# Kernel optimization log

Measured on AMD Instinct MI355X. Metric: run time of the kernel, lower is better.

## Reference

```python
import jax, jax.numpy as jnp
import numpy as np

IN_FEATURES = 1024
OUT_FEATURES = 1024
NUM_TOKENS = 1024
RANK = 32


def setup_inputs() -> dict:
    key = jax.random.key(0)
    ks = jax.random.split(key, 7)
    std = 1.0 / np.sqrt(IN_FEATURES)
    x = jax.random.normal(ks[0], (4, 2048, IN_FEATURES), dtype=jnp.float32)
    key_tokens = std * jax.random.normal(ks[1], (NUM_TOKENS, IN_FEATURES), dtype=jnp.float32)
    value_tokens = std * jax.random.normal(ks[2], (NUM_TOKENS, OUT_FEATURES), dtype=jnp.float32)
    key_down = std * jax.random.normal(ks[3], (IN_FEATURES, RANK), dtype=jnp.float32)
    key_up = std * jax.random.normal(ks[4], (RANK, IN_FEATURES), dtype=jnp.float32)
    value_down = std * jax.random.normal(ks[5], (OUT_FEATURES, RANK), dtype=jnp.float32)
    value_up = std * jax.random.normal(ks[6], (RANK, OUT_FEATURES), dtype=jnp.float32)
    return {"x": x, "key_tokens": key_tokens, "value_tokens": value_tokens,
            "key_down": key_down, "key_up": key_up,
            "value_down": value_down, "value_up": value_up}


def _mod_softmax(attn):
    # scale each row by sqrt(last_dim) / ||row||_2, then GELU
    n = attn.shape[-1]
    norm = jnp.sqrt(jnp.sum(attn * attn, axis=-1, keepdims=True))
    return jax.nn.gelu(attn * (jnp.asarray(n, attn.dtype) ** 0.5) / norm, approximate=False)


def reference(x, key_tokens, value_tokens, key_down, key_up, value_down, value_up):
    key_transformed = jax.nn.gelu((key_tokens @ key_down) @ key_up, approximate=False)
    value_transformed = jax.nn.gelu((value_tokens @ value_down) @ value_up, approximate=False)
    combined_keys = jnp.concatenate([key_tokens, key_transformed], axis=0)      # [2T, in]
    combined_values = jnp.concatenate([value_tokens, value_transformed], axis=0)  # [2T, out]
    similarity = jnp.einsum('bsd,td->bst', x, combined_keys)  # [B, S, 2T]
    weights = _mod_softmax(similarity)
    return jnp.einsum('bst,te->bse', weights, combined_values)  # [B, S, out]
```

## Files before the change

kernel.cpp:

```cpp
#include <hip/hip_runtime.h>

#define IN_F 1024
#define OUT_F 1024
#define NT 1024
#define RANK 32
#define M_TOT 8192
#define N2T 2048

typedef __attribute__((ext_vector_type(8))) short short8;
typedef __attribute__((ext_vector_type(4))) float f32x4;
typedef __attribute__((ext_vector_type(8))) unsigned short ushort8;

__device__ __forceinline__ float geluf(float x) {
  return 0.5f * x * (1.0f + erff(x * 0.7071067811865476f));
}
__device__ __forceinline__ unsigned short f2bf(float f) {
  unsigned x = __float_as_uint(f);
  return (unsigned short)((x + 0x7fffu + ((x >> 16) & 1u)) >> 16);
}
__device__ __forceinline__ float bf2f(unsigned short u) {
  return __uint_as_float(((unsigned)u) << 16);
}


__global__ void down_proj_kernel(const float* __restrict__ kt, const float* __restrict__ kd,
                                 const float* __restrict__ vt, const float* __restrict__ vd,
                                 float* __restrict__ tmpK, float* __restrict__ tmpV) {
  __shared__ float rowbuf[IN_F];
  __shared__ float part[8][32];
  const int row = blockIdx.x & (NT - 1);
  const int mat = blockIdx.x >> 10;
  const float* T = mat ? vt : kt;
  const float* D = mat ? vd : kd;
  const int tid = threadIdx.x;
  *(f32x4*)(rowbuf + tid * 4) = *(const f32x4*)(T + (size_t)row * IN_F + tid * 4);
  __syncthreads();
  const int c = tid & 31;
  const int kc = tid >> 5;
  float s = 0.f;
#pragma unroll 4
  for (int k = kc * 128; k < kc * 128 + 128; ++k) s += rowbuf[k] * D[k * RANK + c];
  part[kc][c] = s;
  __syncthreads();
  if (tid < 32) {
    float acc = 0.f;
#pragma unroll
    for (int i = 0; i < 8; ++i) acc += part[i][tid];
    (mat ? tmpV : tmpK)[row * RANK + tid] = acc;
  }
}

__global__ __launch_bounds__(256) void upK_kernel(
    const float* __restrict__ tmpK, const float* __restrict__ key_up,
    unsigned short* __restrict__ Kb) {
  __shared__ float ldsT[32 * 33];
  __shared__ float ldsU[32 * 64];
  const int tid = threadIdx.x;
  const int t0 = (blockIdx.x >> 4) * 32;
  const int d0 = (blockIdx.x & 15) * 64;
  {
    int row = tid >> 3, col = (tid & 7) * 4;
    f32x4 v = *(const f32x4*)(tmpK + (size_t)(t0 + row) * RANK + col);
#pragma unroll
    for (int j = 0; j < 4; ++j) ldsT[row * 33 + col + j] = v[j];
  }
#pragma unroll
  for (int s = 0; s < 2; ++s) {
    int idx = s * 1024 + tid * 4;
    int r = idx >> 6, cc = idx & 63;
    *(f32x4*)(ldsU + idx) = *(const f32x4*)(key_up + (size_t)r * IN_F + d0 + cc);
  }
  __syncthreads();
  const int lane = tid & 63;
  const int w = tid >> 6;
  float acc[8];
#pragma unroll
  for (int i = 0; i < 8; ++i) acc[i] = 0.f;
#pragma unroll
  for (int r = 0; r < RANK; ++r) {
    float wv = ldsU[r * 64 + lane];
#pragma unroll
    for (int i = 0; i < 8; ++i) acc[i] += ldsT[(w * 8 + i) * 33 + r] * wv;
  }
#pragma unroll
  for (int i = 0; i < 8; ++i) {
    int t = t0 + w * 8 + i;
    Kb[(size_t)(NT + t) * IN_F + d0 + lane] = f2bf(geluf(acc[i]));
  }
}

__global__ __launch_bounds__(256) void upV_kernel(
    const float* __restrict__ tmpV, const float* __restrict__ value_up,
    unsigned short* __restrict__ VbT) {
  __shared__ float ldsT[64 * 33];
  __shared__ float ldsU[32 * 32];
  const int tid = threadIdx.x;
  const int t0 = (blockIdx.x >> 5) * 64;
  const int e0 = (blockIdx.x & 31) * 32;
#pragma unroll
  for (int s = 0; s < 2; ++s) {
    int idx = s * 1024 + tid * 4;
    int row = idx >> 5, col = idx & 31;
    f32x4 v = *(const f32x4*)(tmpV + (size_t)(t0 + row) * RANK + col);
#pragma unroll
    for (int j = 0; j < 4; ++j) ldsT[row * 33 + col + j] = v[j];
  }
  {
    int r = tid >> 3, col = (tid & 7) * 4;
    *(f32x4*)(ldsU + r * 32 + col) = *(const f32x4*)(value_up + (size_t)r * OUT_F + e0 + col);
  }
  __syncthreads();
  const int lane = tid & 63;
  const int w = tid >> 6;
  float acc[8];
#pragma unroll
  for (int i = 0; i < 8; ++i) acc[i] = 0.f;
#pragma unroll
  for (int r = 0; r < RANK; ++r) {
    float uv = ldsT[lane * 33 + r];
#pragma unroll
    for (int i = 0; i < 8; ++i) acc[i] += uv * ldsU[r * 32 + w * 8 + i];
  }
#pragma unroll
  for (int i = 0; i < 8; ++i) {
    int e = e0 + w * 8 + i;
    VbT[(size_t)e * N2T + NT + t0 + lane] = f2bf(geluf(acc[i]));
  }
}

__global__ void vcopy_kernel(const float* __restrict__ vt, unsigned short* __restrict__ VbT) {
  __shared__ float tile[64][65];
  int tid = threadIdx.x;
  int bt = blockIdx.x & 15;
  int be = blockIdx.x >> 4;
  int t0 = bt * 64, e0 = be * 64;
#pragma unroll 1
  for (int it = 0; it < 16; ++it) {
    int tt = it * 4 + (tid >> 6);
    int ee = tid & 63;
    tile[tt][ee] = vt[(size_t)(t0 + tt) * OUT_F + e0 + ee];
  }
  __syncthreads();
#pragma unroll 1
  for (int it = 0; it < 16; ++it) {
    int ee = it * 4 + (tid >> 6);
    int tt = tid & 63;
    VbT[(size_t)(e0 + ee) * N2T + t0 + tt] = f2bf(tile[tt][ee]);
  }
}

__global__ void xcast_kernel(const float* __restrict__ x, unsigned short* __restrict__ xb) {
  int base = (blockIdx.x * blockDim.x + threadIdx.x) * 8;
  f32x4 a = *(const f32x4*)(x + base);
  f32x4 b = *(const f32x4*)(x + base + 4);
  ushort8 o;
  o[0] = f2bf(a[0]); o[1] = f2bf(a[1]); o[2] = f2bf(a[2]); o[3] = f2bf(a[3]);
  o[4] = f2bf(b[0]); o[5] = f2bf(b[1]); o[6] = f2bf(b[2]); o[7] = f2bf(b[3]);
  *(ushort8*)(xb + base) = o;
}

__global__ void gelu_kernel(unsigned short* __restrict__ S, const float* __restrict__ rowsq) {
  int base = (blockIdx.x * blockDim.x + threadIdx.x) * 8;
  int row = base >> 11;
  float scale = sqrtf(2048.0f / rowsq[row]);
  ushort8 v = *(const ushort8*)(S + base);
  ushort8 o;
#pragma unroll
  for (int i = 0; i < 8; ++i) o[i] = f2bf(geluf(bf2f(v[i]) * scale));
  *(ushort8*)(S + base) = o;
}

#define BARRB __builtin_amdgcn_s_barrier()

template <int BN, int KDIM, int NDIM, int DO_SIM>
__global__ __launch_bounds__(512, 2) void gemm2p_kernel(
    const unsigned short* __restrict__ A, const unsigned short* __restrict__ Bm,
    void* __restrict__ Cout, float* __restrict__ rowsq) {
  constexpr int NFRAG = BN / 64;
  constexpr int NH = NFRAG / 2;
  constexpr int LB = BN / 128;
  constexpr int ABUFE = 16384;
  constexpr int BBUFE = BN * 64;
  constexpr int nTN = NDIM / BN;
  constexpr int nkt = KDIM / 64;
  __shared__ unsigned short lds[2 * ABUFE + 2 * BBUFE];

  const int tid = threadIdx.x;
  const int l = tid & 63;
  const int wid = tid >> 6;
  const int wr = wid >> 2;
  const int wc = wid & 3;

  const int nwg = gridDim.x;
  const int cpx = nwg >> 3;
  const int wg = (blockIdx.x & 7) * cpx + (blockIdx.x >> 3);
  const int bx = wg % nTN;
  const int by = wg / nTN;
  const int rowBase = by * 256;
  const int colBase = bx * BN;

  const unsigned short* aSrc[2]; int aLds[2];
#pragma unroll
  for (int j = 0; j < 2; ++j) {
    int slot = j * 512 + tid;
    int rin = slot >> 3;
    int cs = (slot & 7) ^ (rin & 7);
    aSrc[j] = A + (size_t)(rowBase + rin) * KDIM + cs * 8;
    aLds[j] = slot * 8;
  }
  const unsigned short* bSrc[LB]; int bLds[LB];
#pragma unroll
  for (int j = 0; j < LB; ++j) {
    int slot = j * 512 + tid;
    int rin = slot >> 3;
    int cs = (slot & 7) ^ (rin & 7);
    bSrc[j] = Bm + (size_t)(colBase + rin) * KDIM + cs * 8;
    bLds[j] = slot * 8;
  }

#define STAGE_A(u, b, kt) { _Pragma("unroll") for (int j = 0; j < 2; ++j) \
    __builtin_amdgcn_global_load_lds( \
      (const __attribute__((address_space(1))) void*)(aSrc[j] + (size_t)(u) * 128 * KDIM + (kt) * 64), \
      (__attribute__((address_space(3))) void*)(lds + (b) * ABUFE + (u) * 8192 + aLds[j]), 16, 0, 0); }
#define STAGE_B(u, b, kt) { _Pragma("unroll") for (int j = 0; j < LB; ++j) \
    __builtin_amdgcn_global_load_lds( \
      (const __attribute__((address_space(1))) void*)(bSrc[j] + (size_t)(u) * (BN / 2) * KDIM + (kt) * 64), \
      (__attribute__((address_space(3))) void*)(lds + 2 * ABUFE + (b) * BBUFE + (u) * (BBUFE / 2) + bLds[j]), 16, 0, 0); }

  const int kb0 = (l >> 4) * 16;
  const int sw = (l & 7) << 4;
  const int lr = l & 15;

  f32x4 acc[8][NFRAG];
#pragma unroll
  for (int m = 0; m < 8; ++m)
#pragma unroll
    for (int n = 0; n < NFRAG; ++n) acc[m][n] = (f32x4){0.f, 0.f, 0.f, 0.f};

  short8 a[4][2], b0[NH][2], b1[NH][2];

#define LDA(mh, bb_) { _Pragma("unroll") for (int i = 0; i < 4; ++i) { \
    int row = ((mh) * 4 + i) * 32 + wr * 16 + lr; \
    const char* pp = (const char*)lds + (bb_) * 32768 + row * 128; \
    a[i][0] = *(const short8*)(pp + ((0 + kb0) ^ sw)); \
    a[i][1] = *(const short8*)(pp + ((64 + kb0) ^ sw)); } }
#define LDB(dst, nh, bb_) { _Pragma("unroll") for (int i = 0; i < NH; ++i) { \
    int row = ((nh) * NH + i) * 64 + wc * 16 + lr; \
    const char* pp = (const char*)lds + 2 * ABUFE * 2 + (bb_) * BBUFE * 2 + row * 128; \
    dst[i][0] = *(const short8*)(pp + ((0 + kb0) ^ sw)); \
    dst[i][1] = *(const short8*)(pp + ((64 + kb0) ^ sw)); } }
#define DO_MFMA(mh, nh, bb) { _Pragma("unroll") for (int kk = 0; kk < 2; ++kk) \
    _Pragma("unroll") for (int i = 0; i < 4; ++i) \
    _Pragma("unroll") for (int nn = 0; nn < NH; ++nn) \
      acc[(mh) * 4 + i][(nh) * NH + nn] = __builtin_amdgcn_mfma_f32_16x16x32_bf16( \
          a[i][kk], bb[nn][kk], acc[(mh) * 4 + i][(nh) * NH + nn], 0, 0, 0); }

  STAGE_A(0, 0, 0); STAGE_A(1, 0, 0); STAGE_B(0, 0, 0); STAGE_B(1, 0, 0);
  STAGE_A(0, 1, 1); STAGE_B(0, 1, 1); STAGE_B(1, 1, 1);
  if constexpr (LB == 2) { asm volatile("s_waitcnt vmcnt(6)" ::: "memory"); }
  else                   { asm volatile("s_waitcnt vmcnt(4)" ::: "memory"); }
  BARRB;

  for (int t = 0; t < nkt; ++t) {
    const int buf = t & 1;
    LDA(0, buf); LDB(b0, 0, buf); LDB(b1, 1, buf);
    if (t + 1 < nkt) STAGE_A(1, buf ^ 1, t + 1);
    BARRB;
    __builtin_amdgcn_s_setprio(1);
    DO_MFMA(0, 0, b0); DO_MFMA(0, 1, b1);
    __builtin_amdgcn_s_setprio(0);
    BARRB;
    LDA(1, buf);
    if (t + 2 < nkt) { STAGE_A(0, buf, t + 2); STAGE_B(0, buf, t + 2); STAGE_B(1, buf, t + 2); }
    BARRB;
    __builtin_amdgcn_s_setprio(1);
    DO_MFMA(1, 1, b1); DO_MFMA(1, 0, b0);
    __builtin_amdgcn_s_setprio(0);
    if constexpr (LB == 2) { asm volatile("s_waitcnt vmcnt(6)" ::: "memory"); }
    else                   { asm volatile("s_waitcnt vmcnt(4)" ::: "memory"); }
    BARRB;
  }

  const int cq = l >> 4;
  const int cc = l & 15;
  if constexpr (DO_SIM) {
    unsigned short* Sb = (unsigned short*)Cout;
#pragma unroll
    for (int m = 0; m < 8; ++m) {
#pragma unroll
      for (int j = 0; j < 4; ++j) {
        int gr = rowBase + m * 32 + wr * 16 + cq * 4 + j;
        float ss = 0.f;
#pragma unroll
        for (int n = 0; n < NFRAG; ++n) {
          float v = acc[m][n][j];
          ss += v * v;
          Sb[(size_t)gr * NDIM + colBase + n * 64 + wc * 16 + cc] = f2bf(v);
        }
        ss += __shfl_xor(ss, 1, 64);
        ss += __shfl_xor(ss, 2, 64);
        ss += __shfl_xor(ss, 4, 64);
        ss += __shfl_xor(ss, 8, 64);
        if (cc == 0) atomicAdd(&rowsq[gr], ss);
      }
    }
  } else {
    float* Co = (float*)Cout;
#pragma unroll
    for (int m = 0; m < 8; ++m) {
#pragma unroll
      for (int j = 0; j < 4; ++j) {
        int gr = rowBase + m * 32 + wr * 16 + cq * 4 + j;
#pragma unroll
        for (int n = 0; n < NFRAG; ++n)
          Co[(size_t)gr * NDIM + colBase + n * 64 + wc * 16 + cc] = acc[m][n][j];
      }
    }
  }
#undef STAGE_A
#undef STAGE_B
#undef LDA
#undef LDB
#undef DO_MFMA
}


extern "C" void kernel_launch(void* const* d_in, const int* in_sizes, int n_in,
                              void* d_out, int out_size, void* d_ws, size_t ws_size,
                              hipStream_t stream) {
  (void)in_sizes; (void)n_in; (void)out_size; (void)ws_size;
  const float* x            = (const float*)d_in[0];
  const float* key_tokens   = (const float*)d_in[1];
  const float* value_tokens = (const float*)d_in[2];
  const float* key_down     = (const float*)d_in[3];
  const float* key_up       = (const float*)d_in[4];
  const float* value_down   = (const float*)d_in[5];
  const float* value_up     = (const float*)d_in[6];

  char* ws = (char*)d_ws;
  unsigned short* xb  = (unsigned short*)(ws);
  unsigned short* Kb  = (unsigned short*)(ws + 16777216);
  unsigned short* VbT = (unsigned short*)(ws + 20971520);
  unsigned short* S   = (unsigned short*)(ws + 25165824);
  float* tmpK  = (float*)(ws + 58720256);
  float* tmpV  = (float*)(ws + 58851328);
  float* rowsq = (float*)(ws + 58982400);

  hipMemsetAsync(rowsq, 0, M_TOT * sizeof(float), stream);
  down_proj_kernel<<<2 * NT, 256, 0, stream>>>(key_tokens, key_down, value_tokens, value_down, tmpK, tmpV);
  xcast_kernel<<<(NT * IN_F) / (256 * 8), 256, 0, stream>>>(key_tokens, Kb);
  upK_kernel<<<512, 256, 0, stream>>>(tmpK, key_up, Kb);
  vcopy_kernel<<<256, 256, 0, stream>>>(value_tokens, VbT);
  upV_kernel<<<512, 256, 0, stream>>>(tmpV, value_up, VbT);
  xcast_kernel<<<(M_TOT * IN_F) / (256 * 8), 256, 0, stream>>>(x, xb);
  gemm2p_kernel<256, IN_F, N2T, 1><<<256, 512, 0, stream>>>(xb, Kb, (void*)S, rowsq);
  gelu_kernel<<<(M_TOT * N2T) / (256 * 8), 256, 0, stream>>>(S, rowsq);
  gemm2p_kernel<128, N2T, OUT_F, 0><<<256, 512, 0, stream>>>(S, VbT, d_out, nullptr);
}
```

Baseline: 147.3 us.

## Fuse norm-scale GELU into second GEMM A-load and merge prep kernels

```diff
diff --git a/kernel.cpp b/kernel.cpp
--- a/kernel.cpp
+++ b/kernel.cpp
@@ -50,14 +50,25 @@
   }
 }
 
-__global__ __launch_bounds__(256) void upK_kernel(
-    const float* __restrict__ tmpK, const float* __restrict__ key_up,
-    unsigned short* __restrict__ Kb) {
+__global__ __launch_bounds__(256) void kprep_kernel(
+    const float* __restrict__ key_tokens, const float* __restrict__ key_up,
+    const float* __restrict__ tmpK, unsigned short* __restrict__ Kb) {
   __shared__ float ldsT[32 * 33];
   __shared__ float ldsU[32 * 64];
   const int tid = threadIdx.x;
-  const int t0 = (blockIdx.x >> 4) * 32;
-  const int d0 = (blockIdx.x & 15) * 64;
+  if (blockIdx.x < 512) {
+    int base = (blockIdx.x * 256 + tid) * 8;
+    f32x4 a = *(const f32x4*)(key_tokens + base);
+    f32x4 b = *(const f32x4*)(key_tokens + base + 4);
+    ushort8 o;
+    o[0] = f2bf(a[0]); o[1] = f2bf(a[1]); o[2] = f2bf(a[2]); o[3] = f2bf(a[3]);
+    o[4] = f2bf(b[0]); o[5] = f2bf(b[1]); o[6] = f2bf(b[2]); o[7] = f2bf(b[3]);
+    *(ushort8*)(Kb + base) = o;
+    return;
+  }
+  const int bid = blockIdx.x - 512;
+  const int t0 = (bid >> 4) * 32;
+  const int d0 = (bid & 15) * 64;
   {
     int row = tid >> 3, col = (tid & 7) * 4;
     f32x4 v = *(const f32x4*)(tmpK + (size_t)(t0 + row) * RANK + col);
@@ -89,14 +100,35 @@
   }
 }
 
-__global__ __launch_bounds__(256) void upV_kernel(
-    const float* __restrict__ tmpV, const float* __restrict__ value_up,
-    unsigned short* __restrict__ VbT) {
-  __shared__ float ldsT[64 * 33];
+__global__ __launch_bounds__(256) void vprep_kernel(
+    const float* __restrict__ vt, const float* __restrict__ value_up,
+    const float* __restrict__ tmpV, unsigned short* __restrict__ VbT) {
+  __shared__ float tile[64][65];
+  const int tid = threadIdx.x;
+  if (blockIdx.x < 256) {
+    int bt = blockIdx.x & 15;
+    int be = blockIdx.x >> 4;
+    int t0 = bt * 64, e0 = be * 64;
+#pragma unroll 1
+    for (int it = 0; it < 16; ++it) {
+      int tt = it * 4 + (tid >> 6);
+      int ee = tid & 63;
+      tile[tt][ee] = vt[(size_t)(t0 + tt) * OUT_F + e0 + ee];
+    }
+    __syncthreads();
+#pragma unroll 1
+    for (int it = 0; it < 16; ++it) {
+      int ee = it * 4 + (tid >> 6);
+      int tt = tid & 63;
+      VbT[(size_t)(e0 + ee) * N2T + t0 + tt] = f2bf(tile[tt][ee]);
+    }
+    return;
+  }
+  const int bid = blockIdx.x - 256;
+  float* ldsT = &tile[0][0];
   __shared__ float ldsU[32 * 32];
-  const int tid = threadIdx.x;
-  const int t0 = (blockIdx.x >> 5) * 64;
-  const int e0 = (blockIdx.x & 31) * 32;
+  const int t0 = (bid >> 5) * 64;
+  const int e0 = (bid & 31) * 32;
 #pragma unroll
   for (int s = 0; s < 2; ++s) {
     int idx = s * 1024 + tid * 4;
@@ -125,27 +157,6 @@
   for (int i = 0; i < 8; ++i) {
     int e = e0 + w * 8 + i;
     VbT[(size_t)e * N2T + NT + t0 + lane] = f2bf(geluf(acc[i]));
-  }
-}
-
-__global__ void vcopy_kernel(const float* __restrict__ vt, unsigned short* __restrict__ VbT) {
-  __shared__ float tile[64][65];
-  int tid = threadIdx.x;
-  int bt = blockIdx.x & 15;
-  int be = blockIdx.x >> 4;
-  int t0 = bt * 64, e0 = be * 64;
-#pragma unroll 1
-  for (int it = 0; it < 16; ++it) {
-    int tt = it * 4 + (tid >> 6);
-    int ee = tid & 63;
-    tile[tt][ee] = vt[(size_t)(t0 + tt) * OUT_F + e0 + ee];
-  }
-  __syncthreads();
-#pragma unroll 1
-  for (int it = 0; it < 16; ++it) {
-    int ee = it * 4 + (tid >> 6);
-    int tt = tid & 63;
-    VbT[(size_t)(e0 + ee) * N2T + t0 + tt] = f2bf(tile[tt][ee]);
   }
 }
 
@@ -157,17 +168,6 @@
   o[0] = f2bf(a[0]); o[1] = f2bf(a[1]); o[2] = f2bf(a[2]); o[3] = f2bf(a[3]);
   o[4] = f2bf(b[0]); o[5] = f2bf(b[1]); o[6] = f2bf(b[2]); o[7] = f2bf(b[3]);
   *(ushort8*)(xb + base) = o;
-}
-
-__global__ void gelu_kernel(unsigned short* __restrict__ S, const float* __restrict__ rowsq) {
-  int base = (blockIdx.x * blockDim.x + threadIdx.x) * 8;
-  int row = base >> 11;
-  float scale = sqrtf(2048.0f / rowsq[row]);
-  ushort8 v = *(const ushort8*)(S + base);
-  ushort8 o;
-#pragma unroll
-  for (int i = 0; i < 8; ++i) o[i] = f2bf(geluf(bf2f(v[i]) * scale));
-  *(ushort8*)(S + base) = o;
 }
 
 #define BARRB __builtin_amdgcn_s_barrier()
@@ -324,6 +324,148 @@
 #undef DO_MFMA
 }
 
+#define FBARR asm volatile("s_barrier" ::: "memory")
+#define FLGKM0 asm volatile("s_waitcnt lgkmcnt(0)" ::: "memory")
+
+__global__ __launch_bounds__(512, 2) void gemm2f_kernel(
+    const unsigned short* __restrict__ S, const float* __restrict__ rowsq,
+    const unsigned short* __restrict__ Bm, float* __restrict__ Co) {
+  constexpr int KDIM = N2T;
+  constexpr int NDIM = OUT_F;
+  constexpr int BN = 128;
+  constexpr int ABUFE = 16384;
+  constexpr int BBUFE = BN * 64;
+  constexpr int nTN = NDIM / BN;
+  constexpr int nkt = KDIM / 64;
+  __shared__ unsigned short lds[2 * ABUFE + 2 * BBUFE];
+
+  const int tid = threadIdx.x;
+  const int l = tid & 63;
+  const int wid = tid >> 6;
+  const int wr = wid >> 2;
+  const int wc = wid & 3;
+
+  const int nwg = gridDim.x;
+  const int cpx = nwg >> 3;
+  const int wg = (blockIdx.x & 7) * cpx + (blockIdx.x >> 3);
+  const int bx = wg % nTN;
+  const int by = wg / nTN;
+  const int rowBase = by * 256;
+  const int colBase = bx * BN;
+
+  const unsigned short* agp[4]; int albyte[4]; float ascale[4];
+#pragma unroll
+  for (int c = 0; c < 4; ++c) {
+    int slot = c * 512 + tid;
+    int rin = slot >> 3;
+    int cch = slot & 7;
+    agp[c] = S + (size_t)(rowBase + rin) * KDIM + cch * 8;
+    albyte[c] = rin * 128 + ((cch * 16) ^ ((rin & 7) << 4));
+    ascale[c] = sqrtf(2048.0f / rowsq[rowBase + rin]);
+  }
+  const unsigned short* bSrc0; int bLds0;
+  {
+    int slot = tid;
+    int rin = slot >> 3;
+    int cs = (slot & 7) ^ (rin & 7);
+    bSrc0 = Bm + (size_t)(colBase + rin) * KDIM + cs * 8;
+    bLds0 = slot * 8;
+  }
+
+#define F_STAGE_B(u, b, kt) \
+    __builtin_amdgcn_global_load_lds( \
+      (const __attribute__((address_space(1))) void*)(bSrc0 + (size_t)(u) * 64 * KDIM + (kt) * 64), \
+      (__attribute__((address_space(3))) void*)(lds + 2 * ABUFE + (b) * BBUFE + (u) * (BBUFE / 2) + bLds0), 16, 0, 0);
+#define F_ALOAD(c, tk) areg##c = *(const ushort8*)(agp[c] + (size_t)(tk) * 64);
+#define F_XFORM(c, tk) { \
+    ushort8 v_ = areg##c; \
+    ushort8 o_; \
+    _Pragma("unroll") for (int i_ = 0; i_ < 8; ++i_) \
+      o_[i_] = f2bf(geluf(bf2f(v_[i_]) * ascale[c])); \
+    *(ushort8*)((char*)lds + (((tk) & 1) * (ABUFE * 2)) + albyte[c]) = o_; }
+
+  const int kb0 = (l >> 4) * 16;
+  const int sw = (l & 7) << 4;
+  const int lr = l & 15;
+
+  f32x4 acc[8][2];
+#pragma unroll
+  for (int m = 0; m < 8; ++m)
+#pragma unroll
+    for (int n = 0; n < 2; ++n) acc[m][n] = (f32x4){0.f, 0.f, 0.f, 0.f};
+
+  short8 a[4][2], b0[2], b1[2];
+  ushort8 areg0, areg1, areg2, areg3;
+
+#define F_LDA(mh, bb_) { _Pragma("unroll") for (int i = 0; i < 4; ++i) { \
+    int row = ((mh) * 4 + i) * 32 + wr * 16 + lr; \
+    const char* pp = (const char*)lds + (bb_) * 32768 + row * 128; \
+    a[i][0] = *(const short8*)(pp + ((0 + kb0) ^ sw)); \
+    a[i][1] = *(const short8*)(pp + ((64 + kb0) ^ sw)); } }
+#define F_LDB(dst, nh, bb_) { \
+    int row = (nh) * 64 + wc * 16 + lr; \
+    const char* pp = (const char*)lds + 2 * ABUFE * 2 + (bb_) * BBUFE * 2 + row * 128; \
+    dst[0] = *(const short8*)(pp + ((0 + kb0) ^ sw)); \
+    dst[1] = *(const short8*)(pp + ((64 + kb0) ^ sw)); }
+#define F_MFMA(mh, nh, bb) { _Pragma("unroll") for (int kk = 0; kk < 2; ++kk) \
+    _Pragma("unroll") for (int i = 0; i < 4; ++i) \
+      acc[(mh) * 4 + i][(nh)] = __builtin_amdgcn_mfma_f32_16x16x32_bf16( \
+          a[i][kk], bb[kk], acc[(mh) * 4 + i][(nh)], 0, 0, 0); }
+
+  F_STAGE_B(0, 0, 0); F_STAGE_B(1, 0, 0);
+  F_ALOAD(0, 0); F_ALOAD(1, 0); F_ALOAD(2, 0); F_ALOAD(3, 0);
+  F_STAGE_B(0, 1, 1); F_STAGE_B(1, 1, 1);
+  asm volatile("s_waitcnt vmcnt(2)" ::: "memory");
+  F_XFORM(0, 0); F_XFORM(1, 0); F_XFORM(2, 0); F_XFORM(3, 0);
+  F_ALOAD(0, 1); F_ALOAD(1, 1);
+  FLGKM0;
+  FBARR;
+
+  for (int t = 0; t < nkt; ++t) {
+    const int buf = t & 1;
+    F_LDA(0, buf); F_LDB(b0, 0, buf); F_LDB(b1, 1, buf);
+    if (t + 1 < nkt) { F_ALOAD(2, t + 1); F_ALOAD(3, t + 1); }
+    FBARR;
+    __builtin_amdgcn_s_setprio(1);
+    F_MFMA(0, 0, b0); F_MFMA(0, 1, b1);
+    __builtin_amdgcn_s_setprio(0);
+    if (t + 1 < nkt) { F_XFORM(0, t + 1); F_XFORM(1, t + 1); }
+    FLGKM0;
+    FBARR;
+    F_LDA(1, buf);
+    if (t + 2 < nkt) {
+      F_STAGE_B(0, buf, t + 2); F_STAGE_B(1, buf, t + 2);
+      F_ALOAD(0, t + 2); F_ALOAD(1, t + 2);
+    }
+    FBARR;
+    __builtin_amdgcn_s_setprio(1);
+    F_MFMA(1, 1, b1); F_MFMA(1, 0, b0);
+    __builtin_amdgcn_s_setprio(0);
+    if (t + 1 < nkt) { F_XFORM(2, t + 1); F_XFORM(3, t + 1); }
+    FLGKM0;
+    FBARR;
+  }
+
+  const int cq = l >> 4;
+  const int cc = l & 15;
+#pragma unroll
+  for (int m = 0; m < 8; ++m) {
+#pragma unroll
+    for (int j = 0; j < 4; ++j) {
+      int gr = rowBase + m * 32 + wr * 16 + cq * 4 + j;
+#pragma unroll
+      for (int n = 0; n < 2; ++n)
+        Co[(size_t)gr * NDIM + colBase + n * 64 + wc * 16 + cc] = acc[m][n][j];
+    }
+  }
+#undef F_STAGE_B
+#undef F_ALOAD
+#undef F_XFORM
+#undef F_LDA
+#undef F_LDB
+#undef F_MFMA
+}
+
 
 extern "C" void kernel_launch(void* const* d_in, const int* in_sizes, int n_in,
                               void* d_out, int out_size, void* d_ws, size_t ws_size,
@@ -348,12 +490,9 @@
 
   hipMemsetAsync(rowsq, 0, M_TOT * sizeof(float), stream);
   down_proj_kernel<<<2 * NT, 256, 0, stream>>>(key_tokens, key_down, value_tokens, value_down, tmpK, tmpV);
-  xcast_kernel<<<(NT * IN_F) / (256 * 8), 256, 0, stream>>>(key_tokens, Kb);
-  upK_kernel<<<512, 256, 0, stream>>>(tmpK, key_up, Kb);
-  vcopy_kernel<<<256, 256, 0, stream>>>(value_tokens, VbT);
-  upV_kernel<<<512, 256, 0, stream>>>(tmpV, value_up, VbT);
+  kprep_kernel<<<1024, 256, 0, stream>>>(key_tokens, key_up, tmpK, Kb);
+  vprep_kernel<<<768, 256, 0, stream>>>(value_tokens, value_up, tmpV, VbT);
   xcast_kernel<<<(M_TOT * IN_F) / (256 * 8), 256, 0, stream>>>(x, xb);
   gemm2p_kernel<256, IN_F, N2T, 1><<<256, 512, 0, stream>>>(xb, Kb, (void*)S, rowsq);
-  gelu_kernel<<<(M_TOT * N2T) / (256 * 8), 256, 0, stream>>>(S, rowsq);
-  gemm2p_kernel<128, N2T, OUT_F, 0><<<256, 512, 0, stream>>>(S, VbT, d_out, nullptr);
-}
+  gemm2f_kernel<<<256, 512, 0, stream>>>(S, rowsq, VbT, (float*)d_out);
+}
```

New measurement: 224.2 us. +52.2%, slower.

## Fuse prep kernels and fold row-norm GELU into similarity GEMM via grid sync

Applied to the files above, without the earlier changes.

```diff
diff --git a/kernel.cpp b/kernel.cpp
--- a/kernel.cpp
+++ b/kernel.cpp
@@ -1,4 +1,5 @@
 #include <hip/hip_runtime.h>
+#include <hip/hip_cooperative_groups.h>
 
 #define IN_F 1024
 #define OUT_F 1024
@@ -25,14 +26,16 @@
 
 __global__ void down_proj_kernel(const float* __restrict__ kt, const float* __restrict__ kd,
                                  const float* __restrict__ vt, const float* __restrict__ vd,
-                                 float* __restrict__ tmpK, float* __restrict__ tmpV) {
+                                 float* __restrict__ tmpK, float* __restrict__ tmpV,
+                                 float* __restrict__ rowsq) {
   __shared__ float rowbuf[IN_F];
   __shared__ float part[8][32];
+  const int tid = threadIdx.x;
+  if (blockIdx.x < 32) rowsq[blockIdx.x * 256 + tid] = 0.f;
   const int row = blockIdx.x & (NT - 1);
   const int mat = blockIdx.x >> 10;
   const float* T = mat ? vt : kt;
   const float* D = mat ? vd : kd;
-  const int tid = threadIdx.x;
   *(f32x4*)(rowbuf + tid * 4) = *(const f32x4*)(T + (size_t)row * IN_F + tid * 4);
   __syncthreads();
   const int c = tid & 31;
@@ -50,124 +53,116 @@
   }
 }
 
-__global__ __launch_bounds__(256) void upK_kernel(
-    const float* __restrict__ tmpK, const float* __restrict__ key_up,
-    unsigned short* __restrict__ Kb) {
-  __shared__ float ldsT[32 * 33];
-  __shared__ float ldsU[32 * 64];
+__global__ __launch_bounds__(256) void prep_all_kernel(
+    const float* __restrict__ x, const float* __restrict__ key_tokens,
+    const float* __restrict__ value_tokens, const float* __restrict__ key_up,
+    const float* __restrict__ value_up, const float* __restrict__ tmpK,
+    const float* __restrict__ tmpV, unsigned short* __restrict__ xb,
+    unsigned short* __restrict__ Kb, unsigned short* __restrict__ VbT) {
+  __shared__ float smem[64 * 65 + 32 * 64];
   const int tid = threadIdx.x;
-  const int t0 = (blockIdx.x >> 4) * 32;
-  const int d0 = (blockIdx.x & 15) * 64;
+  const int bid = blockIdx.x;
+  if (bid < 4608) {
+    const float* src = (bid < 4096) ? x : key_tokens;
+    unsigned short* dst = (bid < 4096) ? xb : Kb;
+    int b = (bid < 4096) ? bid : (bid - 4096);
+    int base = (b * 256 + tid) * 8;
+    f32x4 a = *(const f32x4*)(src + base);
+    f32x4 c = *(const f32x4*)(src + base + 4);
+    ushort8 o;
+    o[0] = f2bf(a[0]); o[1] = f2bf(a[1]); o[2] = f2bf(a[2]); o[3] = f2bf(a[3]);
+    o[4] = f2bf(c[0]); o[5] = f2bf(c[1]); o[6] = f2bf(c[2]); o[7] = f2bf(c[3]);
+    *(ushort8*)(dst + base) = o;
+    return;
+  }
+  if (bid < 5120) {
+    const int b = bid - 4608;
+    float* ldsT = smem;
+    float* ldsU = smem + 64 * 65;
+    const int t0 = (b >> 4) * 32;
+    const int d0 = (b & 15) * 64;
+    {
+      int row = tid >> 3, col = (tid & 7) * 4;
+      f32x4 v = *(const f32x4*)(tmpK + (size_t)(t0 + row) * RANK + col);
+#pragma unroll
+      for (int j = 0; j < 4; ++j) ldsT[row * 33 + col + j] = v[j];
+    }
+#pragma unroll
+    for (int s = 0; s < 2; ++s) {
+      int idx = s * 1024 + tid * 4;
+      int r = idx >> 6, cc = idx & 63;
+      *(f32x4*)(ldsU + idx) = *(const f32x4*)(key_up + (size_t)r * IN_F + d0 + cc);
+    }
+    __syncthreads();
+    const int lane = tid & 63;
+    const int w = tid >> 6;
+    float acc[8];
+#pragma unroll
+    for (int i = 0; i < 8; ++i) acc[i] = 0.f;
+#pragma unroll
+    for (int r = 0; r < RANK; ++r) {
+      float wv = ldsU[r * 64 + lane];
+#pragma unroll
+      for (int i = 0; i < 8; ++i) acc[i] += ldsT[(w * 8 + i) * 33 + r] * wv;
+    }
+#pragma unroll
+    for (int i = 0; i < 8; ++i)
+      Kb[(size_t)(NT + t0 + w * 8 + i) * IN_F + d0 + lane] = f2bf(geluf(acc[i]));
+    return;
+  }
+  if (bid < 5376) {
+    const int b = bid - 5120;
+    float (*tile)[65] = (float (*)[65])smem;
+    int t0 = (b & 15) * 64, e0 = (b >> 4) * 64;
+#pragma unroll 1
+    for (int it = 0; it < 16; ++it) {
+      int tt = it * 4 + (tid >> 6);
+      int ee = tid & 63;
+      tile[tt][ee] = value_tokens[(size_t)(t0 + tt) * OUT_F + e0 + ee];
+    }
+    __syncthreads();
+#pragma unroll 1
+    for (int it = 0; it < 16; ++it) {
+      int ee = it * 4 + (tid >> 6);
+      int tt = tid & 63;
+      VbT[(size_t)(e0 + ee) * N2T + t0 + tt] = f2bf(tile[tt][ee]);
+    }
+    return;
+  }
   {
-    int row = tid >> 3, col = (tid & 7) * 4;
-    f32x4 v = *(const f32x4*)(tmpK + (size_t)(t0 + row) * RANK + col);
-#pragma unroll
-    for (int j = 0; j < 4; ++j) ldsT[row * 33 + col + j] = v[j];
-  }
-#pragma unroll
-  for (int s = 0; s < 2; ++s) {
-    int idx = s * 1024 + tid * 4;
-    int r = idx >> 6, cc = idx & 63;
-    *(f32x4*)(ldsU + idx) = *(const f32x4*)(key_up + (size_t)r * IN_F + d0 + cc);
-  }
-  __syncthreads();
-  const int lane = tid & 63;
-  const int w = tid >> 6;
-  float acc[8];
-#pragma unroll
-  for (int i = 0; i < 8; ++i) acc[i] = 0.f;
-#pragma unroll
-  for (int r = 0; r < RANK; ++r) {
-    float wv = ldsU[r * 64 + lane];
-#pragma unroll
-    for (int i = 0; i < 8; ++i) acc[i] += ldsT[(w * 8 + i) * 33 + r] * wv;
-  }
-#pragma unroll
-  for (int i = 0; i < 8; ++i) {
-    int t = t0 + w * 8 + i;
-    Kb[(size_t)(NT + t) * IN_F + d0 + lane] = f2bf(geluf(acc[i]));
-  }
-}
-
-__global__ __launch_bounds__(256) void upV_kernel(
-    const float* __restrict__ tmpV, const float* __restrict__ value_up,
-    unsigned short* __restrict__ VbT) {
-  __shared__ float ldsT[64 * 33];
-  __shared__ float ldsU[32 * 32];
-  const int tid = threadIdx.x;
-  const int t0 = (blockIdx.x >> 5) * 64;
-  const int e0 = (blockIdx.x & 31) * 32;
-#pragma unroll
-  for (int s = 0; s < 2; ++s) {
-    int idx = s * 1024 + tid * 4;
-    int row = idx >> 5, col = idx & 31;
-    f32x4 v = *(const f32x4*)(tmpV + (size_t)(t0 + row) * RANK + col);
-#pragma unroll
-    for (int j = 0; j < 4; ++j) ldsT[row * 33 + col + j] = v[j];
-  }
-  {
-    int r = tid >> 3, col = (tid & 7) * 4;
-    *(f32x4*)(ldsU + r * 32 + col) = *(const f32x4*)(value_up + (size_t)r * OUT_F + e0 + col);
-  }
-  __syncthreads();
-  const int lane = tid & 63;
-  const int w = tid >> 6;
-  float acc[8];
-#pragma unroll
-  for (int i = 0; i < 8; ++i) acc[i] = 0.f;
-#pragma unroll
-  for (int r = 0; r < RANK; ++r) {
-    float uv = ldsT[lane * 33 + r];
-#pragma unroll
-    for (int i = 0; i < 8; ++i) acc[i] += uv * ldsU[r * 32 + w * 8 + i];
-  }
-#pragma unroll
-  for (int i = 0; i < 8; ++i) {
-    int e = e0 + w * 8 + i;
-    VbT[(size_t)e * N2T + NT + t0 + lane] = f2bf(geluf(acc[i]));
-  }
-}
-
-__global__ void vcopy_kernel(const float* __restrict__ vt, unsigned short* __restrict__ VbT) {
-  __shared__ float tile[64][65];
-  int tid = threadIdx.x;
-  int bt = blockIdx.x & 15;
-  int be = blockIdx.x >> 4;
-  int t0 = bt * 64, e0 = be * 64;
-#pragma unroll 1
-  for (int it = 0; it < 16; ++it) {
-    int tt = it * 4 + (tid >> 6);
-    int ee = tid & 63;
-    tile[tt][ee] = vt[(size_t)(t0 + tt) * OUT_F + e0 + ee];
-  }
-  __syncthreads();
-#pragma unroll 1
-  for (int it = 0; it < 16; ++it) {
-    int ee = it * 4 + (tid >> 6);
-    int tt = tid & 63;
-    VbT[(size_t)(e0 + ee) * N2T + t0 + tt] = f2bf(tile[tt][ee]);
-  }
-}
-
-__global__ void xcast_kernel(const float* __restrict__ x, unsigned short* __restrict__ xb) {
-  int base = (blockIdx.x * blockDim.x + threadIdx.x) * 8;
-  f32x4 a = *(const f32x4*)(x + base);
-  f32x4 b = *(const f32x4*)(x + base + 4);
-  ushort8 o;
-  o[0] = f2bf(a[0]); o[1] = f2bf(a[1]); o[2] = f2bf(a[2]); o[3] = f2bf(a[3]);
-  o[4] = f2bf(b[0]); o[5] = f2bf(b[1]); o[6] = f2bf(b[2]); o[7] = f2bf(b[3]);
-  *(ushort8*)(xb + base) = o;
-}
-
-__global__ void gelu_kernel(unsigned short* __restrict__ S, const float* __restrict__ rowsq) {
-  int base = (blockIdx.x * blockDim.x + threadIdx.x) * 8;
-  int row = base >> 11;
-  float scale = sqrtf(2048.0f / rowsq[row]);
-  ushort8 v = *(const ushort8*)(S + base);
-  ushort8 o;
-#pragma unroll
-  for (int i = 0; i < 8; ++i) o[i] = f2bf(geluf(bf2f(v[i]) * scale));
-  *(ushort8*)(S + base) = o;
+    const int b = bid - 5376;
+    float* ldsT = smem;
+    float* ldsU = smem + 64 * 65;
+    const int t0 = (b >> 5) * 64;
+    const int e0 = (b & 31) * 32;
+#pragma unroll
+    for (int s = 0; s < 2; ++s) {
+      int idx = s * 1024 + tid * 4;
+      int row = idx >> 5, col = idx & 31;
+      f32x4 v = *(const f32x4*)(tmpV + (size_t)(t0 + row) * RANK + col);
+#pragma unroll
+      for (int j = 0; j < 4; ++j) ldsT[row * 33 + col + j] = v[j];
+    }
+    {
+      int r = tid >> 3, col = (tid & 7) * 4;
+      *(f32x4*)(ldsU + r * 32 + col) = *(const f32x4*)(value_up + (size_t)r * OUT_F + e0 + col);
+    }
+    __syncthreads();
+    const int lane = tid & 63;
+    const int w = tid >> 6;
+    float acc[8];
+#pragma unroll
+    for (int i = 0; i < 8; ++i) acc[i] = 0.f;
+#pragma unroll
+    for (int r = 0; r < RANK; ++r) {
+      float uv = ldsT[lane * 33 + r];
+#pragma unroll
+      for (int i = 0; i < 8; ++i) acc[i] += uv * ldsU[r * 32 + w * 8 + i];
+    }
+#pragma unroll
+    for (int i = 0; i < 8; ++i)
+      VbT[(size_t)(e0 + w * 8 + i) * N2T + NT + t0 + lane] = f2bf(geluf(acc[i]));
+  }
 }
 
 #define BARRB __builtin_amdgcn_s_barrier()
@@ -283,7 +278,7 @@
 
   const int cq = l >> 4;
   const int cc = l & 15;
-  if constexpr (DO_SIM) {
+  if constexpr (DO_SIM == 2) {
     unsigned short* Sb = (unsigned short*)Cout;
 #pragma unroll
     for (int m = 0; m < 8; ++m) {
@@ -292,16 +287,25 @@
         int gr = rowBase + m * 32 + wr * 16 + cq * 4 + j;
         float ss = 0.f;
 #pragma unroll
-        for (int n = 0; n < NFRAG; ++n) {
-          float v = acc[m][n][j];
-          ss += v * v;
-          Sb[(size_t)gr * NDIM + colBase + n * 64 + wc * 16 + cc] = f2bf(v);
-        }
+        for (int n = 0; n < NFRAG; ++n) { float v = acc[m][n][j]; ss += v * v; }
         ss += __shfl_xor(ss, 1, 64);
         ss += __shfl_xor(ss, 2, 64);
         ss += __shfl_xor(ss, 4, 64);
         ss += __shfl_xor(ss, 8, 64);
         if (cc == 0) atomicAdd(&rowsq[gr], ss);
+      }
+    }
+    cooperative_groups::this_grid().sync();
+#pragma unroll
+    for (int m = 0; m < 8; ++m) {
+#pragma unroll
+      for (int j = 0; j < 4; ++j) {
+        int gr = rowBase + m * 32 + wr * 16 + cq * 4 + j;
+        float rs = __hip_atomic_load(&rowsq[gr], __ATOMIC_RELAXED, __HIP_MEMORY_SCOPE_AGENT);
+        float scale = sqrtf(2048.0f / rs);
+#pragma unroll
+        for (int n = 0; n < NFRAG; ++n)
+          Sb[(size_t)gr * NDIM + colBase + n * 64 + wc * 16 + cc] = f2bf(geluf(acc[m][n][j] * scale));
       }
     }
   } else {
@@ -346,14 +350,19 @@
   float* tmpV  = (float*)(ws + 58851328);
   float* rowsq = (float*)(ws + 58982400);
 
-  hipMemsetAsync(rowsq, 0, M_TOT * sizeof(float), stream);
-  down_proj_kernel<<<2 * NT, 256, 0, stream>>>(key_tokens, key_down, value_tokens, value_down, tmpK, tmpV);
-  xcast_kernel<<<(NT * IN_F) / (256 * 8), 256, 0, stream>>>(key_tokens, Kb);
-  upK_kernel<<<512, 256, 0, stream>>>(tmpK, key_up, Kb);
-  vcopy_kernel<<<256, 256, 0, stream>>>(value_tokens, VbT);
-  upV_kernel<<<512, 256, 0, stream>>>(tmpV, value_up, VbT);
-  xcast_kernel<<<(M_TOT * IN_F) / (256 * 8), 256, 0, stream>>>(x, xb);
-  gemm2p_kernel<256, IN_F, N2T, 1><<<256, 512, 0, stream>>>(xb, Kb, (void*)S, rowsq);
-  gelu_kernel<<<(M_TOT * N2T) / (256 * 8), 256, 0, stream>>>(S, rowsq);
+  down_proj_kernel<<<2 * NT, 256, 0, stream>>>(key_tokens, key_down, value_tokens, value_down,
+                                               tmpK, tmpV, rowsq);
+  prep_all_kernel<<<5888, 256, 0, stream>>>(x, key_tokens, value_tokens, key_up, value_up,
+                                            tmpK, tmpV, xb, Kb, VbT);
+  {
+    const unsigned short* g1A = xb;
+    const unsigned short* g1B = Kb;
+    void* g1C = (void*)S;
+    float* g1R = rowsq;
+    void* g1args[] = {(void*)&g1A, (void*)&g1B, (void*)&g1C, (void*)&g1R};
+    hipLaunchCooperativeKernel(
+        reinterpret_cast<void*>(&gemm2p_kernel<256, IN_F, N2T, 2>),
+        dim3(256), dim3(512), g1args, 0u, stream);
+  }
   gemm2p_kernel<128, N2T, OUT_F, 0><<<256, 512, 0, stream>>>(S, VbT, d_out, nullptr);
 }
```

Result: slower. 184.7 us (+25.4%).
